# Kernel optimization log

Measured on AMD Instinct MI355X. Metric: run time of the kernel, lower is better.

## Reference

```python
import jax, jax.numpy as jnp
import numpy as np

NHEADS = 4   # attention heads (search_cfg.nheads)
WS = 7       # spatial search window side -> WS*WS candidates per query
PS = 3       # patch size for distance computation (search_cfg.ps)
K = 16       # top-k neighbors kept (search_cfg.k)


def layer_norm_2d(vid, w, b, eps=1e-6):
    # LayerNorm over channel dim at every (t,h,w) location; vid (B,T,C,H,W)
    mu = vid.mean(axis=2, keepdims=True)
    var = vid.var(axis=2, keepdims=True)
    y = (vid - mu) / jnp.sqrt(var + eps)
    return y * w[None, None, :, None, None] + b[None, None, :, None, None]


def conv1x1(vid, w, b):
    # 1x1 ConvQKV projection: vid (B,T,C,H,W), w (O,C)
    return jnp.einsum('btchw,oc->btohw', vid, w) + b[None, None, :, None, None]


def box_sum(x, ps):
    # sum over centered ps x ps patch (zero pad); x (..., H, W)
    r = ps // 2
    H, W = x.shape[-2], x.shape[-1]
    xp = jnp.pad(x, [(0, 0)] * (x.ndim - 2) + [(r, r), (r, r)])
    out = jnp.zeros_like(x)
    ah, aw = x.ndim - 2, x.ndim - 1
    for dy in range(ps):
        for dx in range(ps):
            s = jax.lax.dynamic_slice_in_dim(xp, dy, H, ah)
            s = jax.lax.dynamic_slice_in_dim(s, dx, W, aw)
            out = out + s
    return out


def nl_search(q, k):
    # patch-based non-local search: q,k (B,T,HD,c,H,W)
    B, T, HD, c, H, W = q.shape
    r = WS // 2
    kp = jnp.pad(k, ((0, 0),) * 4 + ((r, r), (r, r)))  # zero pad = invalid candidates score ~0
    offs = jnp.stack(jnp.meshgrid(jnp.arange(WS), jnp.arange(WS), indexing='ij'), -1).reshape(-1, 2)

    @jax.checkpoint
    def step(carry, off):
        dy, dx = off[0], off[1]
        ksh = jax.lax.dynamic_slice(kp, (0, 0, 0, 0, dy, dx), (B, T, HD, c, H, W))
        s = (q * ksh).sum(axis=3)      # pixel inner products (B,T,HD,H,W)
        s = box_sum(s, PS)             # patch inner products
        return carry, s

    _, scores = jax.lax.scan(step, 0, offs)        # (WS*WS,B,T,HD,H,W)
    scores = jnp.moveaxis(scores, 0, -1)           # (B,T,HD,H,W,WS*WS)
    dists, inds = jax.lax.top_k(scores, K)         # top-k neighbors per query
    return dists, inds


def nl_stack(v, weights, inds):
    # gather the K selected neighbor values, weighted; v (B,T,HD,c,H,W)
    B, T, HD, c, H, W = v.shape
    r = WS // 2
    vp = jnp.pad(v, ((0, 0),) * 4 + ((r, r), (r, r)))
    Hp, Wp = H + 2 * r, W + 2 * r
    row = jnp.arange(H)[:, None, None] + inds // WS   # (B,T,HD,H,W,K)
    col = jnp.arange(W)[None, :, None] + inds % WS
    lin = (row * Wp + col).reshape(B, T, HD, 1, H * W * K)
    vf = vp.reshape(B, T, HD, c, Hp * Wp)
    g = jnp.take_along_axis(vf, jnp.broadcast_to(lin, (B, T, HD, c, H * W * K)), axis=-1)
    g = g.reshape(B, T, HD, c, H, W, K)
    g = g * weights[:, :, :, None]                    # weight each neighbor
    # -> (B*T, HD*c, K, H, W) stack for Conv3d projection
    return jnp.transpose(g, (0, 1, 2, 3, 6, 4, 5)).reshape(B * T, HD * c, K, H, W)


def proj3d(stack, w, b):
    # Conv3d(io_dim, io_dim, (K,3,3), stride=(K,1,1), pad=(0,1,1), groups=NHEADS)
    out = jax.lax.conv_general_dilated(
        stack, w, window_strides=(K, 1, 1),
        padding=((0, 0), (1, 1), (1, 1)),
        dimension_numbers=('NCDHW', 'OIDHW', 'NCDHW'),
        feature_group_count=NHEADS)
    return out[:, :, 0] + b[None, :, None, None]


def setup_inputs() -> dict:
    key = jax.random.key(0)
    ks = jax.random.split(key, 8)
    B, T, C, H, W = 1, 4, 128, 96, 96
    sc = 1.0 / np.sqrt(C)
    inp = {
        'vid': jax.random.normal(ks[0], (B, T, C, H, W), jnp.float32),
        'ln_w': jnp.ones((C,), jnp.float32),
        'ln_b': jnp.zeros((C,), jnp.float32),
        'wq': jax.random.normal(ks[1], (C, C), jnp.float32) * sc,
        'bq': jnp.zeros((C,), jnp.float32),
        'wk': jax.random.normal(ks[2], (C, C), jnp.float32) * sc,
        'bk': jnp.zeros((C,), jnp.float32),
        'wv': jax.random.normal(ks[3], (C, C), jnp.float32) * sc,
        'bv': jnp.zeros((C,), jnp.float32),
        'proj_w': jax.random.normal(ks[4], (C, C // NHEADS, K, 3, 3), jnp.float32) * 0.02,
        'proj_b': jnp.zeros((C,), jnp.float32),
    }
    return inp


def reference(vid, ln_w, ln_b, wq, bq, wk, bk, wv, bv, proj_w, proj_b):
    B, T, C, H, W = vid.shape
    x = layer_norm_2d(vid, ln_w, ln_b)
    q = conv1x1(x, wq, bq)
    k = conv1x1(x, wk, bk)
    v = conv1x1(x, wv, bv)
    hd = lambda t: t.reshape(B, T, NHEADS, C // NHEADS, H, W)
    q, k, v = hd(q), hd(k), hd(v)
    dists, inds = nl_search(q, k)                 # k-NN search
    weights = jax.nn.softmax(dists, axis=-1)      # normalize over K
    stack = nl_stack(v, weights, inds)            # neighbor stacking
    out = proj3d(stack, proj_w, proj_b)           # conv projection collapses K
    return out.reshape(B, T, C, H, W)
```

## Files before the change

kernel.cpp:

```cpp
#include <hip/hip_runtime.h>


typedef float  f32x4  __attribute__((ext_vector_type(4)));
typedef __bf16 bf16x8 __attribute__((ext_vector_type(8)));
typedef __bf16 bf16x4 __attribute__((ext_vector_type(4)));

__device__ __forceinline__ float dpp_shr1(float x) {
  return __int_as_float(__builtin_amdgcn_update_dpp(0, __float_as_int(x), 0x111, 0xf, 0xf, false));
}
__device__ __forceinline__ float dpp_shl1(float x) {
  return __int_as_float(__builtin_amdgcn_update_dpp(0, __float_as_int(x), 0x101, 0xf, 0xf, false));
}

__global__ __launch_bounds__(256) void prep_kernel(
    const float* __restrict__ wq, const float* __restrict__ wk, const float* __restrict__ wv,
    const float* __restrict__ pw, float* __restrict__ Wt, __bf16* __restrict__ pwt) {
  int idx = blockIdx.x * 256 + threadIdx.x;
  const int NPW = 4 * 16 * 9 * 32 * 32;
  if (idx < NPW) {
    int i  = idx & 31;
    int ol = (idx >> 5) & 31;
    int d  = (idx >> 10) % 9;
    int r  = (idx >> 10) / 9;
    int kd = r & 15;
    int g  = r >> 4;
    int o  = g * 32 + ol;
    pwt[idx] = (__bf16)pw[((o * 32 + i) * 16 + kd) * 9 + d];
  } else {
    int widx = idx - NPW;
    if (widx < 128 * 384) {
      int o = widx % 384;
      int c = widx / 384;
      const float* __restrict__ src = (o < 128) ? wq : (o < 256 ? wk : wv);
      Wt[widx] = src[(o & 127) * 128 + c];
    }
  }
}

__global__ __launch_bounds__(64) void ln_stats_kernel(
    const float* __restrict__ vid, float* __restrict__ mu, float* __restrict__ rs) {
  int pix = blockIdx.x * 64 + threadIdx.x;
  int f = blockIdx.y;
  const float* __restrict__ vp = vid + (size_t)f * 128 * 9216 + pix;
  float s = 0.f, s2 = 0.f;
  #pragma unroll 8
  for (int c = 0; c < 128; ++c) { float x = vp[(size_t)c * 9216]; s += x; s2 += x * x; }
  float m_ = s * (1.f / 128.f);
  float v_ = fmaxf(s2 * (1.f / 128.f) - m_ * m_, 0.f);
  mu[f * 9216 + pix] = m_;
  rs[f * 9216 + pix] = rsqrtf(v_ + 1e-6f);
}

__global__ __launch_bounds__(512) void qkv_gemm_kernel(
    const float* __restrict__ vid, const float* __restrict__ mu, const float* __restrict__ rs,
    const float* __restrict__ lnw, const float* __restrict__ lnb,
    const float* __restrict__ Wt, const float* __restrict__ bq, const float* __restrict__ bk,
    const float* __restrict__ bv, float* __restrict__ qb, float* __restrict__ kb,
    __bf16* __restrict__ vbbf) {
  __shared__ __align__(16) float Xs[32][128];
  __shared__ __align__(16) float Ws[32][128];
  __shared__ float muL[128], rsL[128], lwS[128], lbS[128];
  int tid = threadIdx.x;
  int mt = blockIdx.y;
  int N0 = blockIdx.x * 128;
  int f  = mt / 72;
  int pf = (mt % 72) * 128;

  if (tid < 128) {
    muL[tid] = mu[f * 9216 + pf + tid];
    rsL[tid] = rs[f * 9216 + pf + tid];
  } else if (tid < 256) {
    int t2 = tid - 128;
    lwS[t2] = lnw[t2];
    lbS[t2] = lnb[t2];
  }

  int tx = tid & 15, ty = tid >> 4;
  int m0 = ty * 4;
  int sm = tid & 127;
  int sk = tid >> 7;
  float acc[4][8];
  #pragma unroll
  for (int a = 0; a < 4; ++a)
    #pragma unroll
    for (int b = 0; b < 8; ++b) acc[a][b] = 0.f;

  const size_t vbase = (size_t)f * 128 * 9216 + pf;
  float xr[8], wr[8];

  #pragma unroll
  for (int it = 0; it < 8; ++it) {
    int kk = sk + 4 * it;
    xr[it] = vid[vbase + (size_t)kk * 9216 + sm];
    wr[it] = Wt[(size_t)kk * 384 + N0 + sm];
  }
  __syncthreads();
  #pragma unroll
  for (int it = 0; it < 8; ++it) {
    int kk = sk + 4 * it;
    Xs[kk][sm] = (xr[it] - muL[sm]) * rsL[sm] * lwS[kk] + lbS[kk];
    Ws[kk][sm] = wr[it];
  }
  __syncthreads();

  for (int kc = 0; kc < 4; ++kc) {
    if (kc < 3) {
      #pragma unroll
      for (int it = 0; it < 8; ++it) {
        int kk = sk + 4 * it;
        int c = (kc + 1) * 32 + kk;
        xr[it] = vid[vbase + (size_t)c * 9216 + sm];
        wr[it] = Wt[(size_t)c * 384 + N0 + sm];
      }
    }
    #pragma unroll 4
    for (int kk = 0; kk < 32; ++kk) {
      float xa[4], wa[8];
      *(float4*)&xa[0] = *(const float4*)&Xs[kk][m0];
      *(float4*)&wa[0] = *(const float4*)&Ws[kk][tx * 4];
      *(float4*)&wa[4] = *(const float4*)&Ws[kk][64 + tx * 4];
      #pragma unroll
      for (int a = 0; a < 4; ++a)
        #pragma unroll
        for (int b = 0; b < 8; ++b)
          acc[a][b] = fmaf(xa[a], wa[b], acc[a][b]);
    }
    if (kc < 3) {
      __syncthreads();
      #pragma unroll
      for (int it = 0; it < 8; ++it) {
        int kk = sk + 4 * it;
        int c = (kc + 1) * 32 + kk;
        Xs[kk][sm] = (xr[it] - muL[sm]) * rsL[sm] * lwS[c] + lbS[c];
        Ws[kk][sm] = wr[it];
      }
      __syncthreads();
    }
  }

  int sel = blockIdx.x;
  int nlo = tx * 4, nhi = 64 + tx * 4;
  int hlo = nlo >> 5, clo = nlo & 31;
  int hhi = nhi >> 5, chi = nhi & 31;
  const float* __restrict__ bias = (sel == 0) ? bq : (sel == 1 ? bk : bv);
  float4 blo = make_float4(bias[nlo], bias[nlo + 1], bias[nlo + 2], bias[nlo + 3]);
  float4 bhi = make_float4(bias[nhi], bias[nhi + 1], bias[nhi + 2], bias[nhi + 3]);
  size_t base_lo = (size_t)(f * 4 + hlo) * 9216 * 32 + clo;
  size_t base_hi = (size_t)(f * 4 + hhi) * 9216 * 32 + chi;
  if (sel < 2) {
    float* __restrict__ dst = (sel == 0) ? qb : kb;
    #pragma unroll
    for (int a = 0; a < 4; ++a) {
      size_t poff = (size_t)(pf + m0 + a) * 32;
      *(float4*)&dst[base_lo + poff] = make_float4(acc[a][0] + blo.x, acc[a][1] + blo.y,
                                                   acc[a][2] + blo.z, acc[a][3] + blo.w);
      *(float4*)&dst[base_hi + poff] = make_float4(acc[a][4] + bhi.x, acc[a][5] + bhi.y,
                                                   acc[a][6] + bhi.z, acc[a][7] + bhi.w);
    }
  } else {
    #pragma unroll
    for (int a = 0; a < 4; ++a) {
      size_t poff = (size_t)(pf + m0 + a) * 32;
      bf16x4 lo4, hi4;
      lo4[0] = (__bf16)(acc[a][0] + blo.x); lo4[1] = (__bf16)(acc[a][1] + blo.y);
      lo4[2] = (__bf16)(acc[a][2] + blo.z); lo4[3] = (__bf16)(acc[a][3] + blo.w);
      hi4[0] = (__bf16)(acc[a][4] + bhi.x); hi4[1] = (__bf16)(acc[a][5] + bhi.y);
      hi4[2] = (__bf16)(acc[a][6] + bhi.z); hi4[3] = (__bf16)(acc[a][7] + bhi.w);
      *(bf16x4*)&vbbf[base_lo + poff] = lo4;
      *(bf16x4*)&vbbf[base_hi + poff] = hi4;
    }
  }
}

__global__ __launch_bounds__(256, 3) void search_kernel(
    const float* __restrict__ qb, const float* __restrict__ kb,
    float* __restrict__ wgtb, int* __restrict__ indb) {
  __shared__ __align__(16) float klds[16 * 22 * 32];
  __shared__ float slds[2][256];
  int tid = threadIdx.x;
  int th = blockIdx.y;
  int tile = blockIdx.x;
  int iy0 = (tile / 7) * 14, ix0 = (tile % 7) * 14;
  const float* __restrict__ kbase = kb + (size_t)th * 9216 * 32;

  #pragma unroll
  for (int it = 0; it < 11; ++it) {
    int i = it * 256 + tid;
    int r = i / 176, rem = i % 176;
    int col = rem >> 3, c4 = rem & 7;
    int gy = iy0 - 4 + r, gx = ix0 - 4 + col;
    float4 val = make_float4(0.f, 0.f, 0.f, 0.f);
    if ((unsigned)gy < 96u && (unsigned)gx < 96u)
      val = *(const float4*)&kbase[(size_t)(gy * 96 + gx) * 32 + c4 * 4];
    int p = r * 22 + col;
    *(float4*)&klds[p * 32 + ((c4 ^ (p & 7)) << 2)] = val;
  }

  int sy = tid >> 4, sx = tid & 15;
  int qy = iy0 - 1 + sy, qx = ix0 - 1 + sx;
  bool qok = (unsigned)qy < 96u && (unsigned)qx < 96u;
  float4 qv[8];
  #pragma unroll
  for (int j = 0; j < 8; ++j) qv[j] = make_float4(0.f, 0.f, 0.f, 0.f);
  if (qok) {
    const float* __restrict__ qp = qb + ((size_t)th * 9216 + qy * 96 + qx) * 32;
    #pragma unroll
    for (int j = 0; j < 8; ++j) qv[j] = *(const float4*)&qp[j * 4];
  }
  bool inner = (sy >= 1) && (sy <= 14) && (sx >= 1) && (sx <= 14) && qok;

  float tv[16]; int tix[16];
  #pragma unroll
  for (int j = 0; j < 16; ++j) { tv[j] = -3.0e38f; tix[j] = 0; }
  __syncthreads();

  #pragma unroll 1
  for (int dy = 0; dy < 7; ++dy) {
    if (dy > 0) {
      if (tid < 176) {
        int col = tid >> 3, c4 = tid & 7;
        int r = dy + 15;
        int gy = iy0 - 4 + r, gx = ix0 - 4 + col;
        float4 val = make_float4(0.f, 0.f, 0.f, 0.f);
        if ((unsigned)gy < 96u && (unsigned)gx < 96u)
          val = *(const float4*)&kbase[(size_t)(gy * 96 + gx) * 32 + c4 * 4];
        int p = (r & 15) * 22 + col;
        *(float4*)&klds[p * 32 + ((c4 ^ (p & 7)) << 2)] = val;
      }
      __syncthreads();
    }
    #pragma unroll 1
    for (int dx = 0; dx < 7; ++dx) {
      int oi = dy * 7 + dx;
      int p = ((sy + dy) & 15) * 22 + (sx + dx);
      const float* __restrict__ kp = &klds[p * 32];
      int sw = p & 7;
      float sdot = 0.f;
      #pragma unroll
      for (int j = 0; j < 8; ++j) {
        float4 kq = *(const float4*)&kp[(j ^ sw) << 2];
        sdot += qv[j].x * kq.x + qv[j].y * kq.y + qv[j].z * kq.z + qv[j].w * kq.w;
      }
      float h = sdot + dpp_shr1(sdot) + dpp_shl1(sdot);
      slds[oi & 1][tid] = h;
      __syncthreads();
      if (inner) {
        const float* __restrict__ sb = slds[oi & 1];
        float sc = h + sb[tid - 16] + sb[tid + 16];
        float cv = sc; int ci = oi;
        #pragma unroll
        for (int j = 0; j < 16; ++j) {
          bool gt = cv > tv[j];
          float mx = fmaxf(tv[j], cv);
          float mn = fminf(tv[j], cv);
          int nt = gt ? ci : tix[j];
          ci = gt ? tix[j] : ci;
          tv[j] = mx; cv = mn; tix[j] = nt;
        }
      }
    }
  }

  if (inner) {
    float mx = tv[0];
    float e[16], ssum = 0.f;
    #pragma unroll
    for (int j = 0; j < 16; ++j) { e[j] = __expf(tv[j] - mx); ssum += e[j]; }
    float inv = 1.f / ssum;
    size_t base = ((size_t)th * 9216 + qy * 96 + qx) * 16;
    #pragma unroll
    for (int j = 0; j < 4; ++j) {
      *(float4*)&wgtb[base + j * 4] =
          make_float4(e[j*4] * inv, e[j*4+1] * inv, e[j*4+2] * inv, e[j*4+3] * inv);
      *(int4*)&indb[base + j * 4] = make_int4(tix[j*4], tix[j*4+1], tix[j*4+2], tix[j*4+3]);
    }
  }
}

__global__ __launch_bounds__(512) void proj_kernel(
    const __bf16* __restrict__ vb, const float* __restrict__ wgtb, const int* __restrict__ indb,
    const __bf16* __restrict__ pwt, const float* __restrict__ pb, float* __restrict__ outp) {
  __shared__ __align__(16) __bf16 Alds[324 * 40];
  __shared__ __align__(16) __bf16 Blds[288 * 40];
  int tid = threadIdx.x;
  int bid = blockIdx.x;
  int wg = (bid & 7) * 72 + (bid >> 3);
  int th = wg / 36;
  int tile = wg % 36;
  int g = th & 3;
  int ty0 = (tile / 6) * 16, tx0 = (tile % 6) * 16;
  int lane = tid & 63, wid = tid >> 6;
  int kg = lane >> 4, lr = lane & 15;

  bool gact = tid < 324;
  int ry = tid / 18, rx = tid % 18;
  int gy = ty0 - 1 + ry, gx = tx0 - 1 + rx;
  bool inb = gact && (unsigned)gy < 96u && (unsigned)gx < 96u;
  const __bf16* __restrict__ vbase = vb + (size_t)th * 9216 * 32;
  size_t pxoff = inb ? (size_t)(gy * 96 + gx) : 0;
  const int*   __restrict__ ibase = indb + ((size_t)th * 9216 + pxoff) * 16;
  const float* __restrict__ wbase = wgtb + ((size_t)th * 9216 + pxoff) * 16;

  f32x4 acc[2][2];
  acc[0][0] = (f32x4)(0.0f); acc[0][1] = (f32x4)(0.0f);
  acc[1][0] = (f32x4)(0.0f); acc[1][1] = (f32x4)(0.0f);

  int4 iw_i = make_int4(0, 0, 0, 0);
  float4 iw_w = make_float4(0.f, 0.f, 0.f, 0.f);
  int4 vr[4];
  vr[0] = vr[1] = vr[2] = vr[3] = make_int4(0, 0, 0, 0);
  float wcur = 0.f;

  if (inb) {
    iw_i = *(const int4*)&ibase[0];
    iw_w = *(const float4*)&wbase[0];
    int ind0 = iw_i.x;
    int ny = gy + ind0 / 7 - 3, nx = gx + ind0 % 7 - 3;
    if ((unsigned)ny < 96u && (unsigned)nx < 96u) {
      const int4* __restrict__ vp = (const int4*)(vbase + (size_t)(ny * 96 + nx) * 32);
      vr[0] = vp[0]; vr[1] = vp[1]; vr[2] = vp[2]; vr[3] = vp[3];
    }
    wcur = iw_w.x;
  }

  for (int kdb = 0; kdb < 4; ++kdb) {
    #pragma unroll
    for (int kb = 0; kb < 4; ++kb) {
      int kd = kdb * 4 + kb;
      __syncthreads();
      if (gact) {
        __bf16 tmp[32];
        #pragma unroll
        for (int wv = 0; wv < 4; ++wv) {
          unsigned uu[4] = {(unsigned)vr[wv].x, (unsigned)vr[wv].y,
                            (unsigned)vr[wv].z, (unsigned)vr[wv].w};
          #pragma unroll
          for (int j2 = 0; j2 < 4; ++j2) {
            float lo = __uint_as_float(uu[j2] << 16);
            float hi = __uint_as_float(uu[j2] & 0xffff0000u);
            tmp[wv * 8 + j2 * 2]     = (__bf16)(lo * wcur);
            tmp[wv * 8 + j2 * 2 + 1] = (__bf16)(hi * wcur);
          }
        }
        __bf16* dst = &Alds[tid * 40];
        *(int4*)&dst[0]  = *(const int4*)&tmp[0];
        *(int4*)&dst[8]  = *(const int4*)&tmp[8];
        *(int4*)&dst[16] = *(const int4*)&tmp[16];
        *(int4*)&dst[24] = *(const int4*)&tmp[24];
      }
      {
        const __bf16* __restrict__ bsrc = pwt + (size_t)(g * 16 + kd) * 9216;
        #pragma unroll
        for (int itb = 0; itb < 3; ++itb) {
          int i = itb * 512 + tid;
          if (i < 1152) {
            int row = i >> 2, c = i & 3;
            *(int4*)&Blds[row * 40 + c * 8] = *(const int4*)&bsrc[row * 32 + c * 8];
          }
        }
      }
      __syncthreads();
      if (kd < 15) {
        int indn; float wn;
        if (kb == 3) {
          if (inb) {
            iw_i = *(const int4*)&ibase[kd + 1];
            iw_w = *(const float4*)&wbase[kd + 1];
          }
          indn = iw_i.x; wn = iw_w.x;
        } else {
          indn = (kb == 0) ? iw_i.y : (kb == 1) ? iw_i.z : iw_i.w;
          wn   = (kb == 0) ? iw_w.y : (kb == 1) ? iw_w.z : iw_w.w;
        }
        vr[0] = vr[1] = vr[2] = vr[3] = make_int4(0, 0, 0, 0);
        if (inb) {
          int ny = gy + indn / 7 - 3, nx = gx + indn % 7 - 3;
          if ((unsigned)ny < 96u && (unsigned)nx < 96u) {
            const int4* __restrict__ vp = (const int4*)(vbase + (size_t)(ny * 96 + nx) * 32);
            vr[0] = vp[0]; vr[1] = vp[1]; vr[2] = vp[2]; vr[3] = vp[3];
          }
        }
        wcur = wn;
      }
      #pragma unroll
      for (int d = 0; d < 9; ++d) {
        int dy = d / 3 - 1, dx = d % 3 - 1;
        bf16x8 b0 = *(const bf16x8*)&Blds[(d * 32 + lr) * 40 + kg * 8];
        bf16x8 b1 = *(const bf16x8*)&Blds[(d * 32 + 16 + lr) * 40 + kg * 8];
        #pragma unroll
        for (int mt = 0; mt < 2; ++mt) {
          int ryy = wid * 2 + mt + 1 + dy;
          int rxx = lr + 1 + dx;
          bf16x8 af = *(const bf16x8*)&Alds[(ryy * 18 + rxx) * 40 + kg * 8];
          acc[mt][0] = __builtin_amdgcn_mfma_f32_16x16x32_bf16(af, b0, acc[mt][0], 0, 0, 0);
          acc[mt][1] = __builtin_amdgcn_mfma_f32_16x16x32_bf16(af, b1, acc[mt][1], 0, 0, 0);
        }
      }
    }
  }

  int x0 = tx0 + kg * 4;
  int f = th >> 2;
  #pragma unroll
  for (int mt = 0; mt < 2; ++mt) {
    int y = ty0 + wid * 2 + mt;
    #pragma unroll
    for (int nt = 0; nt < 2; ++nt) {
      int o = g * 32 + nt * 16 + lr;
      float bias = pb[o];
      float4 res = make_float4(acc[mt][nt][0] + bias, acc[mt][nt][1] + bias,
                               acc[mt][nt][2] + bias, acc[mt][nt][3] + bias);
      *(float4*)&outp[(size_t)(f * 128 + o) * 9216 + y * 96 + x0] = res;
    }
  }
}

extern "C" void kernel_launch(void* const* d_in, const int* in_sizes, int n_in,
                              void* d_out, int out_size, void* d_ws, size_t ws_size,
                              hipStream_t stream) {
  const float* vid = (const float*)d_in[0];
  const float* lnw = (const float*)d_in[1];
  const float* lnb = (const float*)d_in[2];
  const float* wq  = (const float*)d_in[3];
  const float* bq  = (const float*)d_in[4];
  const float* wk  = (const float*)d_in[5];
  const float* bk  = (const float*)d_in[6];
  const float* wv_ = (const float*)d_in[7];
  const float* bv  = (const float*)d_in[8];
  const float* pw  = (const float*)d_in[9];
  const float* pb  = (const float*)d_in[10];
  float* outp = (float*)d_out;

  const size_t SZ_T  = (size_t)16 * 9216 * 32 * 4;
  const size_t SZ_TB = (size_t)16 * 9216 * 32 * 2;
  const size_t SZ_W  = (size_t)16 * 9216 * 16 * 4;
  const size_t SZ_WT = 128 * 384 * 4;
  const size_t SZ_PW = (size_t)4 * 16 * 9 * 32 * 32 * 2;
  const size_t SZ_MU = (size_t)4 * 9216 * 4;

  char* p = (char*)d_ws;
  float* qb = (float*)p;        p += SZ_T;
  float* kb = (float*)p;        p += SZ_T;
  __bf16* vbbf = (__bf16*)p;    p += SZ_TB;
  float* wgtb = (float*)p;      p += SZ_W;
  int*   indb = (int*)p;        p += SZ_W;
  float* Wt = (float*)p;        p += SZ_WT;
  __bf16* pwt = (__bf16*)p;     p += SZ_PW;
  float* mu = (float*)p;        p += SZ_MU;
  float* rs = (float*)p;

  prep_kernel<<<2496, 256, 0, stream>>>(wq, wk, wv_, pw, Wt, pwt);
  ln_stats_kernel<<<dim3(144, 4), 64, 0, stream>>>(vid, mu, rs);
  qkv_gemm_kernel<<<dim3(3, 288), 512, 0, stream>>>(vid, mu, rs, lnw, lnb, Wt, bq, bk, bv,
                                                    qb, kb, vbbf);
  search_kernel<<<dim3(49, 16), 256, 0, stream>>>(qb, kb, wgtb, indb);
  proj_kernel<<<576, 512, 0, stream>>>(vbbf, wgtb, indb, pwt, pb, outp);
}
```

Measured before the change: 229.5 us.

## Halve proj_kernel block size, give each wave four rows, reuse A fragments in registers

After: 261.8 us. 1.14x slower.

```diff
diff --git a/kernel.cpp b/kernel.cpp
--- a/kernel.cpp
+++ b/kernel.cpp
@@ -277,11 +277,11 @@
   }
 }
 
-__global__ __launch_bounds__(512) void proj_kernel(
+__global__ __launch_bounds__(256) void proj_kernel(
     const __bf16* __restrict__ vb, const float* __restrict__ wgtb, const int* __restrict__ indb,
     const __bf16* __restrict__ pwt, const float* __restrict__ pb, float* __restrict__ outp) {
-  __shared__ __align__(16) __bf16 Alds[324 * 40];
-  __shared__ __align__(16) __bf16 Blds[288 * 40];
+  __shared__ __align__(16) __bf16 Alds[324 * 36];
+  __shared__ __align__(16) __bf16 Blds[288 * 36];
   int tid = threadIdx.x;
   int bid = blockIdx.x;
   int wg = (bid & 7) * 72 + (bid >> 3);
@@ -292,35 +292,52 @@
   int lane = tid & 63, wid = tid >> 6;
   int kg = lane >> 4, lr = lane & 15;
 
-  bool gact = tid < 324;
-  int ry = tid / 18, rx = tid % 18;
-  int gy = ty0 - 1 + ry, gx = tx0 - 1 + rx;
-  bool inb = gact && (unsigned)gy < 96u && (unsigned)gx < 96u;
+  bool act1 = tid < 68;
+  int ry0 = tid / 18, rx0 = tid % 18;
+  int py1 = 256 + tid;
+  int ry1 = py1 / 18, rx1 = py1 % 18;
+  int gy0 = ty0 - 1 + ry0, gx0 = tx0 - 1 + rx0;
+  int gy1 = ty0 - 1 + ry1, gx1 = tx0 - 1 + rx1;
+  bool inb0 = (unsigned)gy0 < 96u && (unsigned)gx0 < 96u;
+  bool inb1 = act1 && (unsigned)gy1 < 96u && (unsigned)gx1 < 96u;
   const __bf16* __restrict__ vbase = vb + (size_t)th * 9216 * 32;
-  size_t pxoff = inb ? (size_t)(gy * 96 + gx) : 0;
-  const int*   __restrict__ ibase = indb + ((size_t)th * 9216 + pxoff) * 16;
-  const float* __restrict__ wbase = wgtb + ((size_t)th * 9216 + pxoff) * 16;
-
-  f32x4 acc[2][2];
-  acc[0][0] = (f32x4)(0.0f); acc[0][1] = (f32x4)(0.0f);
-  acc[1][0] = (f32x4)(0.0f); acc[1][1] = (f32x4)(0.0f);
-
-  int4 iw_i = make_int4(0, 0, 0, 0);
-  float4 iw_w = make_float4(0.f, 0.f, 0.f, 0.f);
-  int4 vr[4];
-  vr[0] = vr[1] = vr[2] = vr[3] = make_int4(0, 0, 0, 0);
-  float wcur = 0.f;
-
-  if (inb) {
-    iw_i = *(const int4*)&ibase[0];
-    iw_w = *(const float4*)&wbase[0];
-    int ind0 = iw_i.x;
-    int ny = gy + ind0 / 7 - 3, nx = gx + ind0 % 7 - 3;
+  size_t px0off = inb0 ? (size_t)(gy0 * 96 + gx0) : 0;
+  size_t px1off = inb1 ? (size_t)(gy1 * 96 + gx1) : 0;
+  const int*   __restrict__ ib0 = indb + ((size_t)th * 9216 + px0off) * 16;
+  const float* __restrict__ wb0 = wgtb + ((size_t)th * 9216 + px0off) * 16;
+  const int*   __restrict__ ib1 = indb + ((size_t)th * 9216 + px1off) * 16;
+  const float* __restrict__ wb1 = wgtb + ((size_t)th * 9216 + px1off) * 16;
+
+  f32x4 acc[4][2];
+  #pragma unroll
+  for (int a = 0; a < 4; ++a) { acc[a][0] = (f32x4)(0.0f); acc[a][1] = (f32x4)(0.0f); }
+
+  int4 iwi0 = make_int4(0,0,0,0), iwi1 = make_int4(0,0,0,0);
+  float4 iww0 = make_float4(0.f,0.f,0.f,0.f), iww1 = make_float4(0.f,0.f,0.f,0.f);
+  int4 vr0[4], vr1[4];
+  #pragma unroll
+  for (int j = 0; j < 4; ++j) { vr0[j] = make_int4(0,0,0,0); vr1[j] = make_int4(0,0,0,0); }
+  float wc0 = 0.f, wc1 = 0.f;
+
+  if (inb0) {
+    iwi0 = *(const int4*)&ib0[0];
+    iww0 = *(const float4*)&wb0[0];
+    int ny = gy0 + iwi0.x / 7 - 3, nx = gx0 + iwi0.x % 7 - 3;
     if ((unsigned)ny < 96u && (unsigned)nx < 96u) {
       const int4* __restrict__ vp = (const int4*)(vbase + (size_t)(ny * 96 + nx) * 32);
-      vr[0] = vp[0]; vr[1] = vp[1]; vr[2] = vp[2]; vr[3] = vp[3];
-    }
-    wcur = iw_w.x;
+      vr0[0] = vp[0]; vr0[1] = vp[1]; vr0[2] = vp[2]; vr0[3] = vp[3];
+    }
+    wc0 = iww0.x;
+  }
+  if (inb1) {
+    iwi1 = *(const int4*)&ib1[0];
+    iww1 = *(const float4*)&wb1[0];
+    int ny = gy1 + iwi1.x / 7 - 3, nx = gx1 + iwi1.x % 7 - 3;
+    if ((unsigned)ny < 96u && (unsigned)nx < 96u) {
+      const int4* __restrict__ vp = (const int4*)(vbase + (size_t)(ny * 96 + nx) * 32);
+      vr1[0] = vp[0]; vr1[1] = vp[1]; vr1[2] = vp[2]; vr1[3] = vp[3];
+    }
+    wc1 = iww1.x;
   }
 
   for (int kdb = 0; kdb < 4; ++kdb) {
@@ -328,72 +345,107 @@
     for (int kb = 0; kb < 4; ++kb) {
       int kd = kdb * 4 + kb;
       __syncthreads();
-      if (gact) {
+      {
         __bf16 tmp[32];
         #pragma unroll
         for (int wv = 0; wv < 4; ++wv) {
-          unsigned uu[4] = {(unsigned)vr[wv].x, (unsigned)vr[wv].y,
-                            (unsigned)vr[wv].z, (unsigned)vr[wv].w};
+          unsigned uu[4] = {(unsigned)vr0[wv].x, (unsigned)vr0[wv].y,
+                            (unsigned)vr0[wv].z, (unsigned)vr0[wv].w};
           #pragma unroll
           for (int j2 = 0; j2 < 4; ++j2) {
             float lo = __uint_as_float(uu[j2] << 16);
             float hi = __uint_as_float(uu[j2] & 0xffff0000u);
-            tmp[wv * 8 + j2 * 2]     = (__bf16)(lo * wcur);
-            tmp[wv * 8 + j2 * 2 + 1] = (__bf16)(hi * wcur);
+            tmp[wv * 8 + j2 * 2]     = (__bf16)(lo * wc0);
+            tmp[wv * 8 + j2 * 2 + 1] = (__bf16)(hi * wc0);
           }
         }
-        __bf16* dst = &Alds[tid * 40];
+        __bf16* dst = &Alds[tid * 36];
         *(int4*)&dst[0]  = *(const int4*)&tmp[0];
         *(int4*)&dst[8]  = *(const int4*)&tmp[8];
         *(int4*)&dst[16] = *(const int4*)&tmp[16];
         *(int4*)&dst[24] = *(const int4*)&tmp[24];
       }
+      if (act1) {
+        __bf16 tmp[32];
+        #pragma unroll
+        for (int wv = 0; wv < 4; ++wv) {
+          unsigned uu[4] = {(unsigned)vr1[wv].x, (unsigned)vr1[wv].y,
+                            (unsigned)vr1[wv].z, (unsigned)vr1[wv].w};
+          #pragma unroll
+          for (int j2 = 0; j2 < 4; ++j2) {
+            float lo = __uint_as_float(uu[j2] << 16);
+            float hi = __uint_as_float(uu[j2] & 0xffff0000u);
+            tmp[wv * 8 + j2 * 2]     = (__bf16)(lo * wc1);
+            tmp[wv * 8 + j2 * 2 + 1] = (__bf16)(hi * wc1);
+          }
+        }
+        __bf16* dst = &Alds[(256 + tid) * 36];
+        *(int4*)&dst[0]  = *(const int4*)&tmp[0];
+        *(int4*)&dst[8]  = *(const int4*)&tmp[8];
+        *(int4*)&dst[16] = *(const int4*)&tmp[16];
+        *(int4*)&dst[24] = *(const int4*)&tmp[24];
+      }
       {
         const __bf16* __restrict__ bsrc = pwt + (size_t)(g * 16 + kd) * 9216;
         #pragma unroll
-        for (int itb = 0; itb < 3; ++itb) {
-          int i = itb * 512 + tid;
+        for (int itb = 0; itb < 5; ++itb) {
+          int i = itb * 256 + tid;
           if (i < 1152) {
             int row = i >> 2, c = i & 3;
-            *(int4*)&Blds[row * 40 + c * 8] = *(const int4*)&bsrc[row * 32 + c * 8];
+            *(int4*)&Blds[row * 36 + c * 8] = *(const int4*)&bsrc[row * 32 + c * 8];
           }
         }
       }
       __syncthreads();
       if (kd < 15) {
-        int indn; float wn;
+        int indn0, indn1; float wn0, wn1;
         if (kb == 3) {
-          if (inb) {
-            iw_i = *(const int4*)&ibase[kd + 1];
-            iw_w = *(const float4*)&wbase[kd + 1];
-          }
-          indn = iw_i.x; wn = iw_w.x;
+          if (inb0) { iwi0 = *(const int4*)&ib0[kd + 1]; iww0 = *(const float4*)&wb0[kd + 1]; }
+          if (inb1) { iwi1 = *(const int4*)&ib1[kd + 1]; iww1 = *(const float4*)&wb1[kd + 1]; }
+          indn0 = iwi0.x; wn0 = iww0.x;
+          indn1 = iwi1.x; wn1 = iww1.x;
         } else {
-          indn = (kb == 0) ? iw_i.y : (kb == 1) ? iw_i.z : iw_i.w;
-          wn   = (kb == 0) ? iw_w.y : (kb == 1) ? iw_w.z : iw_w.w;
-        }
-        vr[0] = vr[1] = vr[2] = vr[3] = make_int4(0, 0, 0, 0);
-        if (inb) {
-          int ny = gy + indn / 7 - 3, nx = gx + indn % 7 - 3;
+          indn0 = (kb == 0) ? iwi0.y : (kb == 1) ? iwi0.z : iwi0.w;
+          wn0   = (kb == 0) ? iww0.y : (kb == 1) ? iww0.z : iww0.w;
+          indn1 = (kb == 0) ? iwi1.y : (kb == 1) ? iwi1.z : iwi1.w;
+          wn1   = (kb == 0) ? iww1.y : (kb == 1) ? iww1.z : iww1.w;
+        }
+        #pragma unroll
+        for (int j = 0; j < 4; ++j) { vr0[j] = make_int4(0,0,0,0); vr1[j] = make_int4(0,0,0,0); }
+        if (inb0) {
+          int ny = gy0 + indn0 / 7 - 3, nx = gx0 + indn0 % 7 - 3;
           if ((unsigned)ny < 96u && (unsigned)nx < 96u) {
             const int4* __restrict__ vp = (const int4*)(vbase + (size_t)(ny * 96 + nx) * 32);
-            vr[0] = vp[0]; vr[1] = vp[1]; vr[2] = vp[2]; vr[3] = vp[3];
+            vr0[0] = vp[0]; vr0[1] = vp[1]; vr0[2] = vp[2]; vr0[3] = vp[3];
           }
         }
-        wcur = wn;
-      }
+        if (inb1) {
+          int ny = gy1 + indn1 / 7 - 3, nx = gx1 + indn1 % 7 - 3;
+          if ((unsigned)ny < 96u && (unsigned)nx < 96u) {
+            const int4* __restrict__ vp = (const int4*)(vbase + (size_t)(ny * 96 + nx) * 32);
+            vr1[0] = vp[0]; vr1[1] = vp[1]; vr1[2] = vp[2]; vr1[3] = vp[3];
+          }
+        }
+        wc0 = wn0; wc1 = wn1;
+      }
+      bf16x8 a[6][3];
       #pragma unroll
-      for (int d = 0; d < 9; ++d) {
-        int dy = d / 3 - 1, dx = d % 3 - 1;
-        bf16x8 b0 = *(const bf16x8*)&Blds[(d * 32 + lr) * 40 + kg * 8];
-        bf16x8 b1 = *(const bf16x8*)&Blds[(d * 32 + 16 + lr) * 40 + kg * 8];
-        #pragma unroll
-        for (int mt = 0; mt < 2; ++mt) {
-          int ryy = wid * 2 + mt + 1 + dy;
-          int rxx = lr + 1 + dx;
-          bf16x8 af = *(const bf16x8*)&Alds[(ryy * 18 + rxx) * 40 + kg * 8];
-          acc[mt][0] = __builtin_amdgcn_mfma_f32_16x16x32_bf16(af, b0, acc[mt][0], 0, 0, 0);
-          acc[mt][1] = __builtin_amdgcn_mfma_f32_16x16x32_bf16(af, b1, acc[mt][1], 0, 0, 0);
+      for (int r = 0; r < 6; ++r)
+        #pragma unroll
+        for (int dxi = 0; dxi < 3; ++dxi)
+          a[r][dxi] = *(const bf16x8*)&Alds[((wid * 4 + r) * 18 + lr + dxi) * 36 + kg * 8];
+      #pragma unroll
+      for (int dy2 = 0; dy2 < 3; ++dy2) {
+        #pragma unroll
+        for (int dx2 = 0; dx2 < 3; ++dx2) {
+          int d = dy2 * 3 + dx2;
+          bf16x8 b0 = *(const bf16x8*)&Blds[(d * 32 + lr) * 36 + kg * 8];
+          bf16x8 b1 = *(const bf16x8*)&Blds[(d * 32 + 16 + lr) * 36 + kg * 8];
+          #pragma unroll
+          for (int mt = 0; mt < 4; ++mt) {
+            acc[mt][0] = __builtin_amdgcn_mfma_f32_16x16x32_bf16(a[mt + dy2][dx2], b0, acc[mt][0], 0, 0, 0);
+            acc[mt][1] = __builtin_amdgcn_mfma_f32_16x16x32_bf16(a[mt + dy2][dx2], b1, acc[mt][1], 0, 0, 0);
+          }
         }
       }
     }
@@ -402,8 +454,8 @@
   int x0 = tx0 + kg * 4;
   int f = th >> 2;
   #pragma unroll
-  for (int mt = 0; mt < 2; ++mt) {
-    int y = ty0 + wid * 2 + mt;
+  for (int mt = 0; mt < 4; ++mt) {
+    int y = ty0 + wid * 4 + mt;
     #pragma unroll
     for (int nt = 0; nt < 2; ++nt) {
       int o = g * 32 + nt * 16 + lr;
@@ -454,5 +506,5 @@
   qkv_gemm_kernel<<<dim3(3, 288), 512, 0, stream>>>(vid, mu, rs, lnw, lnb, Wt, bq, bk, bv,
                                                     qb, kb, vbbf);
   search_kernel<<<dim3(49, 16), 256, 0, stream>>>(qb, kb, wgtb, indb);
-  proj_kernel<<<576, 512, 0, stream>>>(vbbf, wgtb, indb, pwt, pb, outp);
-}
+  proj_kernel<<<576, 256, 0, stream>>>(vbbf, wgtb, indb, pwt, pb, outp);
+}
```
